# Kernel tuning notes

Measured on AMD Instinct MI355X. Metric: run time of the kernel, lower is better.

Reference implementation:

```python
import jax, jax.numpy as jnp
import numpy as np
import math


def _per_component_log_likelihood(x, MU, A, D, PI):
    # x: [N,d]; MU,D: [K,d]; A: [K,d,l]; PI: [K]
    K, d, l = A.shape
    iD = D ** (-2.0)                                   # [K,d]  (1/sigma^2 per feature)
    B = iD[:, :, None] * A                             # [K,d,l] = diag(iD_k) @ A_k
    # L_k = I_l + A_k^T diag(iD_k) A_k  (Woodbury inner matrix)
    L = jnp.eye(l, dtype=x.dtype)[None] + jnp.einsum('kdl,kdm->klm', A, B)
    iL = jnp.linalg.inv(L)                             # [K,l,l]
    # Mahalanobis term m_d[n,k] = xc^T iD xc - (xc^T iD A) iL (A^T iD xc),
    # expanded so we never materialize the [K,N,d] centered tensor.
    t_quad = (x * x) @ iD.T                            # [N,K]
    t_cross = x @ (iD * MU).T                          # [N,K]
    t_const = jnp.sum(iD * MU * MU, axis=1)            # [K]
    term1 = t_quad - 2.0 * t_cross + t_const[None, :]
    y = jnp.einsum('nd,kdl->nkl', x, B) - jnp.einsum('kd,kdl->kl', MU, B)[None]
    term2 = jnp.einsum('nkl,klm,nkm->nk', y, iL, y)
    m_d = term1 - term2                                # [N,K]
    # log|Sigma_k| = log|L_k| - sum_d log iD[k,d]
    log_det_Sigma = jnp.log(jnp.linalg.det(L)) + jnp.sum(jnp.log(D ** 2.0), axis=1)
    log_prob = -0.5 * ((d * math.log(2.0 * math.pi) + log_det_Sigma)[None, :] + m_d)
    # NOTE: faithful to the source, which adds PI (not log PI) here.
    return PI[None, :] + log_prob                      # [N,K]


def setup_inputs() -> dict:
    key = jax.random.key(0)
    k1, k2, k3, k4 = jax.random.split(key, 4)
    N, K, d, l = 500000, 32, 128, 4
    x = jax.random.normal(k1, (N, d), dtype=jnp.float32)
    MU = jax.random.normal(k2, (K, d), dtype=jnp.float32)
    A = 0.1 * jax.random.normal(k3, (K, d, l), dtype=jnp.float32)
    D = jax.random.uniform(k4, (K, d), dtype=jnp.float32, minval=0.5, maxval=1.5)
    PI = jnp.ones((K,), dtype=jnp.float32) / K
    return {"x": x, "MU": MU, "A": A, "D": D, "PI": PI}


def reference(x, MU, A, D, PI):
    comp_ll = _per_component_log_likelihood(x, MU, A, D, PI)   # [N,K]
    return jax.scipy.special.logsumexp(comp_ll, axis=1)        # [N] = MFA.log_prob(x)
```

## Files before the change

### kernel.cpp

```cpp
#include <hip/hip_runtime.h>
#include <hip/hip_bf16.h>

typedef _Float16 half8 __attribute__((ext_vector_type(8)));
typedef float f32x4 __attribute__((ext_vector_type(4)));

#define KC 32
#define DD 128
#define LL 4
#define NCOL 192
#define EPS 164
#define NBLK 256

__global__ __launch_bounds__(256) void mfa_precompute(
    const float* __restrict__ MU, const float* __restrict__ A,
    const float* __restrict__ D, const float* __restrict__ PI,
    _Float16* __restrict__ wsw, float* __restrict__ wsc, float* __restrict__ wsh)
{
  __shared__ float sPart[KC][8][16];
  __shared__ float sRi[KC][LL][LL];
  const int tid = threadIdx.x;
  const int k = tid >> 3;
  const int sub = tid & 7;

  {
    float p[16];
#pragma unroll
    for (int i = 0; i < 16; ++i) p[i] = 0.f;
    const int d0 = sub * 16;
    for (int di = 0; di < 16; ++di) {
      const int d = d0 + di;
      const float Dv = D[k*DD + d];
      const float id = 1.0f/(Dv*Dv);
      const float mu = MU[k*DD + d];
      float a[LL];
#pragma unroll
      for (int l = 0; l < LL; ++l) a[l] = A[(k*DD + d)*LL + l];
      int s = 0;
#pragma unroll
      for (int l = 0; l < LL; ++l) {
#pragma unroll
        for (int m2 = 0; m2 <= l; ++m2) { p[s] += a[l]*id*a[m2]; ++s; }
        p[10 + l] += mu*id*a[l];
      }
      p[14] += id*mu*mu;
      p[15] += logf(Dv*Dv);
    }
#pragma unroll
    for (int i = 0; i < 16; ++i) sPart[k][sub][i] = p[i];
  }
  __syncthreads();

  if (tid < KC) {
    const int kk = tid;
    float p[16];
#pragma unroll
    for (int i = 0; i < 16; ++i) p[i] = 0.f;
    for (int s = 0; s < 8; ++s)
#pragma unroll
      for (int i = 0; i < 16; ++i) p[i] += sPart[kk][s][i];

    float Lm[LL][LL];
    {
      int s = 0;
      for (int l = 0; l < LL; ++l)
        for (int m2 = 0; m2 <= l; ++m2) { Lm[l][m2] = p[s]; ++s; }
    }
    for (int l = 0; l < LL; ++l) Lm[l][l] += 1.0f;
    float c[LL];
    for (int l = 0; l < LL; ++l) c[l] = p[10 + l];
    const float t_const  = p[14];
    const float sumlogD2 = p[15];

    float Lo[LL][LL];
    for (int i = 0; i < LL; ++i)
      for (int j = 0; j < LL; ++j) Lo[i][j] = 0.f;
    for (int i = 0; i < LL; ++i) {
      float s = Lm[i][i];
      for (int m2 = 0; m2 < i; ++m2) s -= Lo[i][m2]*Lo[i][m2];
      Lo[i][i] = sqrtf(s);
      for (int j = i + 1; j < LL; ++j) {
        float t = Lm[j][i];
        for (int m2 = 0; m2 < i; ++m2) t -= Lo[j][m2]*Lo[i][m2];
        Lo[j][i] = t / Lo[i][i];
      }
    }
    float Ri[LL][LL];
    for (int i = 0; i < LL; ++i)
      for (int j = 0; j < LL; ++j) Ri[i][j] = 0.f;
    for (int i = 0; i < LL; ++i) {
      Ri[i][i] = 1.0f/Lo[i][i];
      for (int j = 0; j < i; ++j) {
        float s = 0.f;
        for (int m2 = j; m2 < i; ++m2) s += Lo[i][m2]*Ri[m2][j];
        Ri[i][j] = -s / Lo[i][i];
      }
    }
    for (int i = 0; i < LL; ++i)
      for (int j = 0; j < LL; ++j) sRi[kk][i][j] = Ri[i][j];
    for (int l = 0; l < LL; ++l) {
      float s = 0.f;
      for (int m2 = 0; m2 <= l; ++m2) s += Ri[l][m2]*c[m2];
      wsh[kk*LL + l] = s;
    }
    float logdetL = 0.f;
    for (int i = 0; i < LL; ++i) logdetL += logf(Lo[i][i]);
    logdetL *= 2.0f;
    const float dlog2pi = 235.24826473f;
    wsc[kk] = PI[kk] - 0.5f*(dlog2pi + logdetL + sumlogD2) - 0.5f*t_const;
  }
  __syncthreads();

  for (int idx = tid; idx < NCOL*DD; idx += blockDim.x) {
    const int j8   = idx & 7;
    const int lane = (idx >> 3) & 63;
    const int s    = (idx >> 9) & 3;
    const int t    = idx >> 11;
    const int col  = t*16 + (lane & 15);
    const int dd   = s*32 + ((lane >> 4) << 3) + j8;
    float v;
    if (col < 32) {
      const float Dv = D[col*DD + dd];
      v = 1.0f/(Dv*Dv);
    } else if (col < 64) {
      const int kk = col - 32;
      const float Dv = D[kk*DD + dd];
      v = MU[kk*DD + dd]/(Dv*Dv);
    } else {
      const int kk = (col - 64) >> 2, l = (col - 64) & 3;
      const float Dv = D[kk*DD + dd];
      const float id = 1.0f/(Dv*Dv);
      float s2 = 0.f;
      for (int m2 = 0; m2 <= l; ++m2) s2 += A[(kk*DD + dd)*LL + m2]*sRi[kk][l][m2];
      v = id*s2;
    }
    wsw[idx] = (_Float16)v;
  }
}

__global__ __launch_bounds__(256) void mfa_main(
    const float* __restrict__ x, const _Float16* __restrict__ wsw,
    const float* __restrict__ wsc, const float* __restrict__ wsh,
    float* __restrict__ out, int N, int ntiles, int iters)
{
  __shared__ int4 sWbuf[3072];
  __shared__ alignas(16) float sC[KC];
  __shared__ alignas(16) float sH[KC*LL];
  __shared__ alignas(16) float sEp[4][16*EPS];
  const int tid = threadIdx.x;

  {
    const int4* src = (const int4*)wsw;
    for (int i = tid; i < 3072; i += 256) sWbuf[i] = src[i];
    if (tid < KC) sC[tid] = wsc[tid];
    if (tid < KC*LL) sH[tid] = wsh[tid];
  }
  __syncthreads();

  const half8* sW8 = (const half8*)sWbuf;
  const int wv = tid >> 6, lane = tid & 63;
  const int m = lane & 15, g = lane >> 4;
  float* ep = &sEp[wv][0];

  for (int it = 0; it < iters; ++it) {
    const int tile = it*(NBLK*4) + (int)blockIdx.x*4 + wv;
    const bool valid = tile < ntiles;
    f32x4 acc[12];

    if (valid) {
      int row = tile*16 + m;
      if (row >= N) row = N - 1;
      const float* xr = x + (size_t)row*DD + g*8;
      half8 ax[4], ax2[4];
#pragma unroll
      for (int s = 0; s < 4; ++s) {
        const float4 v0 = *(const float4*)(xr + s*32);
        const float4 v1 = *(const float4*)(xr + s*32 + 4);
        half8 h, h2;
        h[0] = (_Float16)v0.x; h[1] = (_Float16)v0.y;
        h[2] = (_Float16)v0.z; h[3] = (_Float16)v0.w;
        h[4] = (_Float16)v1.x; h[5] = (_Float16)v1.y;
        h[6] = (_Float16)v1.z; h[7] = (_Float16)v1.w;
        h2[0] = (_Float16)(v0.x*v0.x); h2[1] = (_Float16)(v0.y*v0.y);
        h2[2] = (_Float16)(v0.z*v0.z); h2[3] = (_Float16)(v0.w*v0.w);
        h2[4] = (_Float16)(v1.x*v1.x); h2[5] = (_Float16)(v1.y*v1.y);
        h2[6] = (_Float16)(v1.z*v1.z); h2[7] = (_Float16)(v1.w*v1.w);
        ax[s] = h; ax2[s] = h2;
      }
#pragma unroll
      for (int t = 0; t < 12; ++t)
#pragma unroll
        for (int r = 0; r < 4; ++r) acc[t][r] = 0.f;

#pragma unroll
      for (int s = 0; s < 4; ++s) {
#pragma unroll
        for (int t = 0; t < 12; ++t) {
          const half8 b = sW8[(t*4 + s)*64 + lane];
          acc[t] = __builtin_amdgcn_mfma_f32_16x16x32_f16(
              (t < 2) ? ax2[s] : ax[s], b, acc[t], 0, 0, 0);
        }
      }
    }

    __syncthreads();

    if (valid) {
      f32x4 u0, u1;
#pragma unroll
      for (int r = 0; r < 4; ++r) {
        u0[r] = acc[2][r] - 0.5f*acc[0][r];
        u1[r] = acc[3][r] - 0.5f*acc[1][r];
      }
#pragma unroll
      for (int r = 0; r < 4; ++r) {
        ep[(g*4 + r)*EPS + m]       = u0[r];
        ep[(g*4 + r)*EPS + 16 + m]  = u1[r];
      }
#pragma unroll
      for (int t = 4; t < 12; ++t)
#pragma unroll
        for (int r = 0; r < 4; ++r)
          ep[(g*4 + r)*EPS + 32 + (t - 4)*16 + m] = acc[t][r];
    }

    __syncthreads();

    if (valid) {
      const float* eprow = ep + m*EPS;
      float ll[8];
      float lmax = -3.0e38f;
#pragma unroll
      for (int i = 0; i < 8; ++i) {
        const int k = g*8 + i;
        const float u = eprow[k];
        const float4 z = *(const float4*)(eprow + 32 + 4*k);
        const float4 h = *(const float4*)(sH + 4*k);
        const float z0 = z.x - h.x, z1 = z.y - h.y;
        const float z2 = z.z - h.z, z3 = z.w - h.w;
        const float t2 = z0*z0 + z1*z1 + z2*z2 + z3*z3;
        const float v = sC[k] + u + 0.5f*t2;
        ll[i] = v;
        lmax = fmaxf(lmax, v);
      }
      lmax = fmaxf(lmax, __shfl_xor(lmax, 16));
      lmax = fmaxf(lmax, __shfl_xor(lmax, 32));
      float sum = 0.f;
#pragma unroll
      for (int i = 0; i < 8; ++i) sum += __expf(ll[i] - lmax);
      sum += __shfl_xor(sum, 16);
      sum += __shfl_xor(sum, 32);
      if (g == 0) {
        const int n = tile*16 + m;
        if (n < N) out[n] = lmax + __logf(sum);
      }
    }
  }
}

extern "C" void kernel_launch(void* const* d_in, const int* in_sizes, int n_in,
                              void* d_out, int out_size, void* d_ws, size_t ws_size,
                              hipStream_t stream) {
  const float* x  = (const float*)d_in[0];
  const float* MU = (const float*)d_in[1];
  const float* A  = (const float*)d_in[2];
  const float* D  = (const float*)d_in[3];
  const float* PI = (const float*)d_in[4];
  float* out = (float*)d_out;

  const int N = in_sizes[0] / DD;
  _Float16* wsw = (_Float16*)d_ws;
  float* wsc = (float*)((char*)d_ws + (size_t)NCOL*DD*sizeof(_Float16));
  float* wsh = wsc + KC;

  hipLaunchKernelGGL(mfa_precompute, dim3(1), dim3(256), 0, stream,
                     MU, A, D, PI, wsw, wsc, wsh);

  const int ntiles = (N + 15) / 16;
  const int iters  = (ntiles + NBLK*4 - 1) / (NBLK*4);
  hipLaunchKernelGGL(mfa_main, dim3(NBLK), dim3(256), 0, stream,
                     x, wsw, wsc, wsh, out, N, ntiles, iters);
}
```

Measured before the change: 422.0 us.

## Move logsumexp epilogue into registers via lane shuffles, drop LDS staging and barriers

The per-tile epilogue no longer writes MFMA accumulators to shared memory and reads them back behind two block-wide barriers. It instead reduces the Woodbury quadratic terms and the logsumexp across lanes with cross-lane shuffles, and each wave writes a float4 of results. Per-component constants are held in registers. The grid grows to 768 blocks and the kernel requests 3 blocks per CU, so waves run independently with more occupancy. The cost is extra shuffle instructions and dropping the row clamp, which assumes N is a multiple of 16.

```diff
diff --git a/kernel.cpp b/kernel.cpp
--- a/kernel.cpp
+++ b/kernel.cpp
@@ -8,8 +8,7 @@
 #define DD 128
 #define LL 4
 #define NCOL 192
-#define EPS 164
-#define NBLK 256
+#define NBLK 768
 
 __global__ __launch_bounds__(256) void mfa_precompute(
     const float* __restrict__ MU, const float* __restrict__ A,
@@ -137,122 +136,114 @@
   }
 }
 
-__global__ __launch_bounds__(256) void mfa_main(
+__global__ __launch_bounds__(256, 3) void mfa_main(
     const float* __restrict__ x, const _Float16* __restrict__ wsw,
     const float* __restrict__ wsc, const float* __restrict__ wsh,
     float* __restrict__ out, int N, int ntiles, int iters)
 {
   __shared__ int4 sWbuf[3072];
-  __shared__ alignas(16) float sC[KC];
-  __shared__ alignas(16) float sH[KC*LL];
-  __shared__ alignas(16) float sEp[4][16*EPS];
   const int tid = threadIdx.x;
 
   {
     const int4* src = (const int4*)wsw;
     for (int i = tid; i < 3072; i += 256) sWbuf[i] = src[i];
-    if (tid < KC) sC[tid] = wsc[tid];
-    if (tid < KC*LL) sH[tid] = wsh[tid];
-  }
-  __syncthreads();
+  }
 
   const half8* sW8 = (const half8*)sWbuf;
   const int wv = tid >> 6, lane = tid & 63;
   const int m = lane & 15, g = lane >> 4;
-  float* ep = &sEp[wv][0];
+  const int q = m >> 2;
+  const int gbase = lane & 48;
+
+  const float c0 = wsc[m];
+  const float c1 = wsc[16 + m];
+  float hh[8];
+#pragma unroll
+  for (int j = 0; j < 8; ++j) hh[j] = wsh[j*16 + m];
+
+  __syncthreads();
 
   for (int it = 0; it < iters; ++it) {
     const int tile = it*(NBLK*4) + (int)blockIdx.x*4 + wv;
-    const bool valid = tile < ntiles;
+    if (tile >= ntiles) continue;
+
+    const int row = tile*16 + m;
+    const float* xr = x + (size_t)row*DD + g*8;
+    half8 ax[4], ax2[4];
+#pragma unroll
+    for (int s = 0; s < 4; ++s) {
+      const float4 v0 = *(const float4*)(xr + s*32);
+      const float4 v1 = *(const float4*)(xr + s*32 + 4);
+      half8 h, h2;
+      h[0] = (_Float16)v0.x; h[1] = (_Float16)v0.y;
+      h[2] = (_Float16)v0.z; h[3] = (_Float16)v0.w;
+      h[4] = (_Float16)v1.x; h[5] = (_Float16)v1.y;
+      h[6] = (_Float16)v1.z; h[7] = (_Float16)v1.w;
+      h2[0] = (_Float16)(v0.x*v0.x); h2[1] = (_Float16)(v0.y*v0.y);
+      h2[2] = (_Float16)(v0.z*v0.z); h2[3] = (_Float16)(v0.w*v0.w);
+      h2[4] = (_Float16)(v1.x*v1.x); h2[5] = (_Float16)(v1.y*v1.y);
+      h2[6] = (_Float16)(v1.z*v1.z); h2[7] = (_Float16)(v1.w*v1.w);
+      ax[s] = h; ax2[s] = h2;
+    }
+
     f32x4 acc[12];
-
-    if (valid) {
-      int row = tile*16 + m;
-      if (row >= N) row = N - 1;
-      const float* xr = x + (size_t)row*DD + g*8;
-      half8 ax[4], ax2[4];
-#pragma unroll
-      for (int s = 0; s < 4; ++s) {
-        const float4 v0 = *(const float4*)(xr + s*32);
-        const float4 v1 = *(const float4*)(xr + s*32 + 4);
-        half8 h, h2;
-        h[0] = (_Float16)v0.x; h[1] = (_Float16)v0.y;
-        h[2] = (_Float16)v0.z; h[3] = (_Float16)v0.w;
-        h[4] = (_Float16)v1.x; h[5] = (_Float16)v1.y;
-        h[6] = (_Float16)v1.z; h[7] = (_Float16)v1.w;
-        h2[0] = (_Float16)(v0.x*v0.x); h2[1] = (_Float16)(v0.y*v0.y);
-        h2[2] = (_Float16)(v0.z*v0.z); h2[3] = (_Float16)(v0.w*v0.w);
-        h2[4] = (_Float16)(v1.x*v1.x); h2[5] = (_Float16)(v1.y*v1.y);
-        h2[6] = (_Float16)(v1.z*v1.z); h2[7] = (_Float16)(v1.w*v1.w);
-        ax[s] = h; ax2[s] = h2;
-      }
-#pragma unroll
-      for (int t = 0; t < 12; ++t)
-#pragma unroll
-        for (int r = 0; r < 4; ++r) acc[t][r] = 0.f;
-
-#pragma unroll
-      for (int s = 0; s < 4; ++s) {
-#pragma unroll
-        for (int t = 0; t < 12; ++t) {
-          const half8 b = sW8[(t*4 + s)*64 + lane];
-          acc[t] = __builtin_amdgcn_mfma_f32_16x16x32_f16(
-              (t < 2) ? ax2[s] : ax[s], b, acc[t], 0, 0, 0);
-        }
-      }
-    }
-
-    __syncthreads();
-
-    if (valid) {
-      f32x4 u0, u1;
+#pragma unroll
+    for (int t = 0; t < 12; ++t)
+#pragma unroll
+      for (int r = 0; r < 4; ++r) acc[t][r] = 0.f;
+
+#pragma unroll
+    for (int s = 0; s < 4; ++s) {
+#pragma unroll
+      for (int t = 0; t < 12; ++t) {
+        const half8 b = sW8[(t*4 + s)*64 + lane];
+        acc[t] = __builtin_amdgcn_mfma_f32_16x16x32_f16(
+            (t < 2) ? ax2[s] : ax[s], b, acc[t], 0, 0, 0);
+      }
+    }
+
+    float vp0[4], vp1[4];
+#pragma unroll
+    for (int r = 0; r < 4; ++r) {
+      vp0[r] = acc[2][r] - 0.5f*acc[0][r] + c0;
+      vp1[r] = acc[3][r] - 0.5f*acc[1][r] + c1;
+    }
+    float t2[8][4];
+#pragma unroll
+    for (int j = 0; j < 8; ++j)
 #pragma unroll
       for (int r = 0; r < 4; ++r) {
-        u0[r] = acc[2][r] - 0.5f*acc[0][r];
-        u1[r] = acc[3][r] - 0.5f*acc[1][r];
-      }
-#pragma unroll
-      for (int r = 0; r < 4; ++r) {
-        ep[(g*4 + r)*EPS + m]       = u0[r];
-        ep[(g*4 + r)*EPS + 16 + m]  = u1[r];
-      }
-#pragma unroll
-      for (int t = 4; t < 12; ++t)
-#pragma unroll
-        for (int r = 0; r < 4; ++r)
-          ep[(g*4 + r)*EPS + 32 + (t - 4)*16 + m] = acc[t][r];
-    }
-
-    __syncthreads();
-
-    if (valid) {
-      const float* eprow = ep + m*EPS;
-      float ll[8];
-      float lmax = -3.0e38f;
-#pragma unroll
-      for (int i = 0; i < 8; ++i) {
-        const int k = g*8 + i;
-        const float u = eprow[k];
-        const float4 z = *(const float4*)(eprow + 32 + 4*k);
-        const float4 h = *(const float4*)(sH + 4*k);
-        const float z0 = z.x - h.x, z1 = z.y - h.y;
-        const float z2 = z.z - h.z, z3 = z.w - h.w;
-        const float t2 = z0*z0 + z1*z1 + z2*z2 + z3*z3;
-        const float v = sC[k] + u + 0.5f*t2;
-        ll[i] = v;
-        lmax = fmaxf(lmax, v);
-      }
-      lmax = fmaxf(lmax, __shfl_xor(lmax, 16));
-      lmax = fmaxf(lmax, __shfl_xor(lmax, 32));
+        float e = acc[j + 4][r] - hh[j];
+        e = e*e;
+        e += __shfl_xor(e, 1);
+        e += __shfl_xor(e, 2);
+        t2[j][r] = e;
+      }
+    float res[4];
+#pragma unroll
+    for (int r = 0; r < 4; ++r) {
+      float v[8];
+#pragma unroll
+      for (int jj = 0; jj < 4; ++jj) {
+        const int src = gbase + 4*jj + q;
+        v[jj]     = __shfl(vp0[r], src) + 0.5f*t2[jj][r];
+        v[jj + 4] = __shfl(vp1[r], src) + 0.5f*t2[jj + 4][r];
+      }
+      float mx = v[0];
+#pragma unroll
+      for (int i = 1; i < 8; ++i) mx = fmaxf(mx, v[i]);
+      mx = fmaxf(mx, __shfl_xor(mx, 4));
+      mx = fmaxf(mx, __shfl_xor(mx, 8));
       float sum = 0.f;
 #pragma unroll
-      for (int i = 0; i < 8; ++i) sum += __expf(ll[i] - lmax);
-      sum += __shfl_xor(sum, 16);
-      sum += __shfl_xor(sum, 32);
-      if (g == 0) {
-        const int n = tile*16 + m;
-        if (n < N) out[n] = lmax + __logf(sum);
-      }
+      for (int i = 0; i < 8; ++i) sum += __expf(v[i] - mx);
+      sum += __shfl_xor(sum, 4);
+      sum += __shfl_xor(sum, 8);
+      res[r] = mx + __logf(sum);
+    }
+    if (m == 0) {
+      float4 o; o.x = res[0]; o.y = res[1]; o.z = res[2]; o.w = res[3];
+      *(float4*)(out + (size_t)tile*16 + g*4) = o;
     }
   }
 }
```

Result: faster. 401.6 us (-4.8%).
